# Kernel tuning notes

Hardware: AMD Instinct MI355X
Metric: run time of the kernel (lower is better)

Reference implementation:

```python
import jax, jax.numpy as jnp
import numpy as np

NE = 64        # num experts
H = 1024       # hidden_size
F = 2048       # ffn_hidden_size per expert
T = 16384      # total tokens


def setup_inputs() -> dict:
    key = jax.random.key(0)
    k1, k2, k3 = jax.random.split(key, 3)
    x = jax.random.normal(k1, (T, H), jnp.float32)
    w1 = jax.random.normal(k2, (NE, F, H), jnp.float32) * 0.02
    w2 = jax.random.normal(k3, (NE, F, H), jnp.float32) * 0.02
    # ragged token counts per expert, summing exactly to T
    rng = np.random.default_rng(0)
    sizes = rng.multinomial(T, np.ones(NE) / NE)
    tokens_per_expert = jnp.asarray(sizes, jnp.int32)
    return {"x": x, "w1": w1, "w2": w2, "tokens_per_expert": tokens_per_expert}


def _grouped_gmm(x, w, sizes, trans_b=False):
    # grouped GEMM: per-expert segment of x multiplied by that expert's weight.
    # sizes are concrete host ints (group boundaries are static), so we emit
    # one GEMM per expert with static slices, matching gg.ops.gmm semantics.
    offs = np.concatenate([[0], np.cumsum(sizes)]).astype(np.int64)
    outs = []
    for e in range(len(sizes)):
        xe = x[int(offs[e]):int(offs[e + 1])]          # [n_e, k]
        we = w[e].T if trans_b else w[e]               # [k, n]
        outs.append(xe @ we)
    return jnp.concatenate(outs, axis=0)


def reference(x, w1, w2, tokens_per_expert):
    sizes = np.asarray(tokens_per_expert)
    h = _grouped_gmm(x, w1, sizes, trans_b=True)       # [T, F]
    h = jax.nn.gelu(h, approximate=False)              # torch F.gelu (exact erf)
    return _grouped_gmm(h, w2, sizes, trans_b=False)   # [T, H]
```

## Files before the change

### kernel.cpp

```cpp
#include <hip/hip_runtime.h>
#include <hip/hip_bf16.h>

#define NE 64
#define HDIM 1024
#define FDIM 2048
#define TDIM 16384

typedef __attribute__((ext_vector_type(8))) short short8;
typedef __attribute__((ext_vector_type(4))) float f32x4;
typedef unsigned short u16;
typedef unsigned int u32;

__device__ __forceinline__ u16 f2bf(float f) {
  return __bfloat16_as_ushort(__float2bfloat16(f));
}
__device__ __forceinline__ u32 pk2(float a, float b) {
  return (u32)f2bf(a) | ((u32)f2bf(b) << 16);
}

__global__ void k_prep(const int* __restrict__ tpe, int4* __restrict__ map,
                       int* __restrict__ nblocks) {
  if (threadIdx.x != 0 || blockIdx.x != 0) return;
  int off = 0, nb = 0;
  for (int e = 0; e < NE; ++e) {
    int n = tpe[e];
    for (int r = 0; r < n; r += 128) {
      int re = (r + 128 < n) ? (r + 128) : n;
      map[nb++] = make_int4(e, off + r, off + re, 0);
    }
    off += n;
  }
  *nblocks = nb;
}

__global__ void k_conv(const float4* __restrict__ in, uint2* __restrict__ out, int n4) {
  int stride = gridDim.x * blockDim.x;
  for (int i = blockIdx.x * blockDim.x + threadIdx.x; i < n4; i += stride) {
    float4 v = in[i];
    uint2 o;
    o.x = pk2(v.x, v.y);
    o.y = pk2(v.z, v.w);
    out[i] = o;
  }
}

template<int K, int N, bool GELU, int BMODE>
__global__ __launch_bounds__(256) void k_gemm(
    const u16* __restrict__ A, const float* __restrict__ Bf, void* __restrict__ C,
    const int4* __restrict__ map, const int* __restrict__ nblocks)
{
  if ((int)blockIdx.x >= *nblocks) return;
  const int4 mi = map[blockIdx.x];
  const int e = mi.x, row0 = mi.y, rowend = mi.z;
  const int n0 = blockIdx.y << 7;
  const int NT = K / 32;

  __shared__ u16 sa[2][4096];
  __shared__ u16 sb[2][128 * 40];

  const int tid = threadIdx.x;
  const int wid = tid >> 6, lane = tid & 63;
  const int wr = wid >> 1, wc = wid & 1;
  const int fr = lane & 15, fq = lane >> 4;

  f32x4 acc[4][4];
#pragma unroll
  for (int m = 0; m < 4; ++m)
#pragma unroll
    for (int n = 0; n < 4; ++n) acc[m][n] = (f32x4)0.f;

  const float* B = Bf + (size_t)e * ((size_t)N * K);

  float4 v1[4];
  float2 v2[8];
  const int np2 = (tid & 63) << 1;
  const int oct = tid >> 6;

  auto issueA = [&](int t, int buf) {
#pragma unroll
    for (int i = 0; i < 2; ++i) {
      int slot = i * 256 + tid;
      int row = row0 + (slot >> 2);
      row = row < TDIM ? row : TDIM - 1;
      const u16* g = A + (size_t)row * K + t * 32 + (slot & 3) * 8;
      __builtin_amdgcn_global_load_lds(
          (const __attribute__((address_space(1))) u32*)g,
          (__attribute__((address_space(3))) u32*)(&sa[buf][i * 2048 + wid * 512]),
          16, 0, 0);
    }
  };
  auto loadB = [&](int t) {
    if constexpr (BMODE == 1) {
#pragma unroll
      for (int i = 0; i < 4; ++i) {
        int slot = i * 256 + tid;
        v1[i] = *(const float4*)(B + (size_t)(n0 + (slot >> 3)) * K + t * 32 + (slot & 7) * 4);
      }
    } else {
      const float* src = B + (size_t)(t * 32 + oct * 8) * N + n0 + np2;
#pragma unroll
      for (int i = 0; i < 8; ++i) v2[i] = *(const float2*)(src + (size_t)i * N);
    }
  };
  auto writeB = [&](int buf) {
    if constexpr (BMODE == 1) {
#pragma unroll
      for (int i = 0; i < 4; ++i) {
        int slot = i * 256 + tid;
        uint2 o;
        o.x = pk2(v1[i].x, v1[i].y);
        o.y = pk2(v1[i].z, v1[i].w);
        *(uint2*)(&sb[buf][(slot >> 3) * 40 + (slot & 7) * 4]) = o;
      }
    } else {
      uint4 c0, c1;
      c0.x = pk2(v2[0].x, v2[1].x); c0.y = pk2(v2[2].x, v2[3].x);
      c0.z = pk2(v2[4].x, v2[5].x); c0.w = pk2(v2[6].x, v2[7].x);
      c1.x = pk2(v2[0].y, v2[1].y); c1.y = pk2(v2[2].y, v2[3].y);
      c1.z = pk2(v2[4].y, v2[5].y); c1.w = pk2(v2[6].y, v2[7].y);
      *(uint4*)(&sb[buf][np2 * 40 + oct * 8]) = c0;
      *(uint4*)(&sb[buf][(np2 + 1) * 40 + oct * 8]) = c1;
    }
  };

  issueA(0, 0);
  loadB(0);
  writeB(0);
  __syncthreads();

  for (int t = 0; t < NT; ++t) {
    const int cur = t & 1, nxt = cur ^ 1;
    if (t + 1 < NT) {
      issueA(t + 1, nxt);
      loadB(t + 1);
    }
    short8 av[4], bv[4];
#pragma unroll
    for (int m = 0; m < 4; ++m)
      av[m] = *(const short8*)(&sa[cur][(wr * 64 + m * 16 + fr) * 32 + fq * 8]);
#pragma unroll
    for (int n = 0; n < 4; ++n)
      bv[n] = *(const short8*)(&sb[cur][(wc * 64 + n * 16 + fr) * 40 + fq * 8]);
#pragma unroll
    for (int m = 0; m < 4; ++m)
#pragma unroll
      for (int n = 0; n < 4; ++n)
        acc[m][n] = __builtin_amdgcn_mfma_f32_16x16x32_bf16(av[m], bv[n], acc[m][n], 0, 0, 0);
    if (t + 1 < NT) writeB(nxt);
    __syncthreads();
  }

#pragma unroll
  for (int m = 0; m < 4; ++m) {
    const int rb = row0 + wr * 64 + m * 16 + fq * 4;
#pragma unroll
    for (int n = 0; n < 4; ++n) {
      const int col = n0 + wc * 64 + n * 16 + fr;
#pragma unroll
      for (int j = 0; j < 4; ++j) {
        int r = rb + j;
        if (r < rowend) {
          float vv = acc[m][n][j];
          if constexpr (GELU) {
            vv = 0.5f * vv * (1.f + erff(vv * 0.70710678118654752f));
            ((u16*)C)[(size_t)r * N + col] = f2bf(vv);
          } else {
            ((float*)C)[(size_t)r * N + col] = vv;
          }
        }
      }
    }
  }
}

extern "C" void kernel_launch(void* const* d_in, const int* in_sizes, int n_in,
                              void* d_out, int out_size, void* d_ws, size_t ws_size,
                              hipStream_t stream) {
  const float* x  = (const float*)d_in[0];
  const float* w1 = (const float*)d_in[1];
  const float* w2 = (const float*)d_in[2];
  const int*  tpe = (const int*)d_in[3];

  char* ws = (char*)d_ws;
  int4* map     = (int4*)ws;
  int*  nblocks = (int*)(ws + 4096);
  u16*  xb      = (u16*)(ws + 8192);
  u16*  hb      = xb + (size_t)TDIM * HDIM;

  k_prep<<<1, 64, 0, stream>>>(tpe, map, nblocks);
  k_conv<<<2048, 256, 0, stream>>>((const float4*)x, (uint2*)xb, (TDIM * HDIM) / 4);
  k_gemm<HDIM, FDIM, true,  1><<<dim3(192, FDIM / 128), 256, 0, stream>>>(
      xb, w1, (void*)hb, map, nblocks);
  k_gemm<FDIM, HDIM, false, 2><<<dim3(192, HDIM / 128), 256, 0, stream>>>(
      hb, w2, d_out, map, nblocks);
}
```

Measured before the change: 560.3 us.

## Deepen GEMM prefetch pipeline with register double-buffered B and manual waitcnt

Restructures the grouped-GEMM main loop into a deeper software pipeline. A tiles are issued via direct-to-LDS loads two steps ahead. Fp32 B tiles are prefetched three steps ahead into two alternating register sets, then converted and written to a now single-buffered B shared-memory tile. Explicit s_waitcnt vmcnt/lgkmcnt and split s_barrier calls replace __syncthreads, with sched_barrier fencing, so global-load latency is hidden behind the MFMA work. The trade-offs are higher register pressure and hand-tuned vmcnt counts. Those counts may not cover the tail iterations where fewer loads are outstanding, which could let the last A tile be read before it has fully arrived.

```diff
diff --git a/kernel.cpp b/kernel.cpp
--- a/kernel.cpp
+++ b/kernel.cpp
@@ -11,11 +11,23 @@
 typedef unsigned short u16;
 typedef unsigned int u32;
 
+struct IC0 { static constexpr int v = 0; };
+struct IC1 { static constexpr int v = 1; };
+
 __device__ __forceinline__ u16 f2bf(float f) {
   return __bfloat16_as_ushort(__float2bfloat16(f));
 }
 __device__ __forceinline__ u32 pk2(float a, float b) {
   return (u32)f2bf(a) | ((u32)f2bf(b) << 16);
+}
+template<int N> __device__ __forceinline__ void waitv() {
+  if constexpr (N == 4)       asm volatile("s_waitcnt vmcnt(4)" ::: "memory");
+  else if constexpr (N == 6)  asm volatile("s_waitcnt vmcnt(6)" ::: "memory");
+  else if constexpr (N == 8)  asm volatile("s_waitcnt vmcnt(8)" ::: "memory");
+  else if constexpr (N == 10) asm volatile("s_waitcnt vmcnt(10)" ::: "memory");
+}
+__device__ __forceinline__ void waitl() {
+  asm volatile("s_waitcnt lgkmcnt(0)" ::: "memory");
 }
 
 __global__ void k_prep(const int* __restrict__ tpe, int4* __restrict__ map,
@@ -54,9 +66,10 @@
   const int e = mi.x, row0 = mi.y, rowend = mi.z;
   const int n0 = blockIdx.y << 7;
   const int NT = K / 32;
+  constexpr int LB = (BMODE == 1) ? 4 : 8;
 
   __shared__ u16 sa[2][4096];
-  __shared__ u16 sb[2][128 * 40];
+  __shared__ u16 sb[128 * 40];
 
   const int tid = threadIdx.x;
   const int wid = tid >> 6, lane = tid & 63;
@@ -71,12 +84,13 @@
 
   const float* B = Bf + (size_t)e * ((size_t)N * K);
 
-  float4 v1[4];
-  float2 v2[8];
+  float4 rb1[2][4];
+  float2 rb2[2][8];
   const int np2 = (tid & 63) << 1;
   const int oct = tid >> 6;
 
-  auto issueA = [&](int t, int buf) {
+  auto issueA = [&](int t) {
+    const int buf = t & 1;
 #pragma unroll
     for (int i = 0; i < 2; ++i) {
       int slot = i * 256 + tid;
@@ -89,65 +103,78 @@
           16, 0, 0);
     }
   };
-  auto loadB = [&](int t) {
+  auto loadB = [&](int t, auto ic) {
+    constexpr int S = decltype(ic)::v;
     if constexpr (BMODE == 1) {
 #pragma unroll
       for (int i = 0; i < 4; ++i) {
         int slot = i * 256 + tid;
-        v1[i] = *(const float4*)(B + (size_t)(n0 + (slot >> 3)) * K + t * 32 + (slot & 7) * 4);
+        rb1[S][i] = *(const float4*)(B + (size_t)(n0 + (slot >> 3)) * K + t * 32 + (slot & 7) * 4);
       }
     } else {
       const float* src = B + (size_t)(t * 32 + oct * 8) * N + n0 + np2;
 #pragma unroll
-      for (int i = 0; i < 8; ++i) v2[i] = *(const float2*)(src + (size_t)i * N);
-    }
-  };
-  auto writeB = [&](int buf) {
+      for (int i = 0; i < 8; ++i) rb2[S][i] = *(const float2*)(src + (size_t)i * N);
+    }
+  };
+  auto writeB = [&](auto ic) {
+    constexpr int S = decltype(ic)::v;
     if constexpr (BMODE == 1) {
 #pragma unroll
       for (int i = 0; i < 4; ++i) {
         int slot = i * 256 + tid;
         uint2 o;
-        o.x = pk2(v1[i].x, v1[i].y);
-        o.y = pk2(v1[i].z, v1[i].w);
-        *(uint2*)(&sb[buf][(slot >> 3) * 40 + (slot & 7) * 4]) = o;
+        o.x = pk2(rb1[S][i].x, rb1[S][i].y);
+        o.y = pk2(rb1[S][i].z, rb1[S][i].w);
+        *(uint2*)(&sb[(slot >> 3) * 40 + (slot & 7) * 4]) = o;
       }
     } else {
       uint4 c0, c1;
-      c0.x = pk2(v2[0].x, v2[1].x); c0.y = pk2(v2[2].x, v2[3].x);
-      c0.z = pk2(v2[4].x, v2[5].x); c0.w = pk2(v2[6].x, v2[7].x);
-      c1.x = pk2(v2[0].y, v2[1].y); c1.y = pk2(v2[2].y, v2[3].y);
-      c1.z = pk2(v2[4].y, v2[5].y); c1.w = pk2(v2[6].y, v2[7].y);
-      *(uint4*)(&sb[buf][np2 * 40 + oct * 8]) = c0;
-      *(uint4*)(&sb[buf][(np2 + 1) * 40 + oct * 8]) = c1;
-    }
-  };
-
-  issueA(0, 0);
-  loadB(0);
-  writeB(0);
-  __syncthreads();
-
-  for (int t = 0; t < NT; ++t) {
-    const int cur = t & 1, nxt = cur ^ 1;
-    if (t + 1 < NT) {
-      issueA(t + 1, nxt);
-      loadB(t + 1);
-    }
+      c0.x = pk2(rb2[S][0].x, rb2[S][1].x); c0.y = pk2(rb2[S][2].x, rb2[S][3].x);
+      c0.z = pk2(rb2[S][4].x, rb2[S][5].x); c0.w = pk2(rb2[S][6].x, rb2[S][7].x);
+      c1.x = pk2(rb2[S][0].y, rb2[S][1].y); c1.y = pk2(rb2[S][2].y, rb2[S][3].y);
+      c1.z = pk2(rb2[S][4].y, rb2[S][5].y); c1.w = pk2(rb2[S][6].y, rb2[S][7].y);
+      *(uint4*)(&sb[np2 * 40 + oct * 8]) = c0;
+      *(uint4*)(&sb[(np2 + 1) * 40 + oct * 8]) = c1;
+    }
+  };
+
+  auto body = [&](int t, auto icCur) {
+    waitv<2 + LB>();
+    waitl();
+    __builtin_amdgcn_s_barrier();
+    const int cur = t & 1;
     short8 av[4], bv[4];
 #pragma unroll
     for (int m = 0; m < 4; ++m)
       av[m] = *(const short8*)(&sa[cur][(wr * 64 + m * 16 + fr) * 32 + fq * 8]);
 #pragma unroll
     for (int n = 0; n < 4; ++n)
-      bv[n] = *(const short8*)(&sb[cur][(wc * 64 + n * 16 + fr) * 40 + fq * 8]);
+      bv[n] = *(const short8*)(&sb[(wc * 64 + n * 16 + fr) * 40 + fq * 8]);
+    waitl();
+    __builtin_amdgcn_sched_barrier(0);
+    __builtin_amdgcn_s_barrier();
+    if (t + 2 < NT) issueA(t + 2);
+    if (t + 1 < NT) writeB(icCur);
+    if (t + 3 < NT) loadB(t + 3, icCur);
+    __builtin_amdgcn_sched_barrier(0);
 #pragma unroll
     for (int m = 0; m < 4; ++m)
 #pragma unroll
       for (int n = 0; n < 4; ++n)
         acc[m][n] = __builtin_amdgcn_mfma_f32_16x16x32_bf16(av[m], bv[n], acc[m][n], 0, 0, 0);
-    if (t + 1 < NT) writeB(nxt);
-    __syncthreads();
+  };
+
+  issueA(0);
+  loadB(0, IC0{});
+  loadB(1, IC1{});
+  waitv<LB>();
+  writeB(IC0{});
+  issueA(1);
+  loadB(2, IC0{});
+  for (int t = 0; t < NT; t += 2) {
+    body(t, IC1{});
+    body(t + 1, IC0{});
   }
 
 #pragma unroll
```

Measured after the change: 555.0 us. No clear change (-0.9%).
